# Kernel tuning notes

Hardware: AMD Instinct MI355X
Metric: run time of the kernel (lower is better)

## Reference

```python
import jax, jax.numpy as jnp
import numpy as np

EPS = 1e-10

def _iou(a, b):
    """IoU for boxes in (cx, cy, w, h) format; a, b: (..., 4)."""
    a_min = a[..., :2] - a[..., 2:] * 0.5
    a_max = a[..., :2] + a[..., 2:] * 0.5
    b_min = b[..., :2] - b[..., 2:] * 0.5
    b_max = b[..., :2] + b[..., 2:] * 0.5
    inter_wh = jnp.clip(jnp.minimum(a_max, b_max) - jnp.maximum(a_min, b_min), 0.0)
    inter = inter_wh[..., 0] * inter_wh[..., 1]
    area_a = a[..., 2] * a[..., 3]
    area_b = b[..., 2] * b[..., 3]
    return inter / (area_a + area_b - inter + EPS)

def setup_inputs() -> dict:
    key = jax.random.key(0)
    k1, k2, k3 = jax.random.split(key, 3)
    BATCH, S, C = 16384, 7, 30
    # uniform in (0.01, 1) so sqrt() of w,h channels is finite/differentiable
    preds = jax.random.uniform(k1, (BATCH, S, S, C), jnp.float32, 0.01, 1.0)
    labels = jax.random.uniform(k2, (BATCH, S, S, C), jnp.float32, 0.01, 1.0)
    obj = jax.random.bernoulli(k3, 0.15, (BATCH, S, S)).astype(jnp.float32)
    labels = labels.at[..., 4].set(obj)  # code branches on labels[...,4] == 1
    return {"preds": preds, "labels": labels}

def reference(preds, labels):
    batch = preds.shape[0]
    obj = labels[..., 4] == 1.0  # (B, S, S)
    # faithful quirk: label bbox x-coord is read transposed (labels[i, y, x, 0])
    lb0 = jnp.swapaxes(labels[..., 0], 1, 2)
    lbox = jnp.stack([lb0, labels[..., 1], labels[..., 2], labels[..., 3]], axis=-1)
    iou1 = _iou(preds[..., 0:4], lbox)
    iou2 = _iou(preds[..., 5:9], lbox)
    choose1 = iou1 > iou2
    # branch where box 1 is responsible
    b1 = (5.0 * jnp.sum((preds[..., 0:2] - labels[..., 0:2]) ** 2, -1)
          + jnp.sum((jnp.sqrt(preds[..., 2:4]) - jnp.sqrt(labels[..., 2:4])) ** 2, -1)
          + (iou1 - preds[..., 4]) ** 2
          + 0.5 * preds[..., 9] ** 2)
    # branch where box 2 is responsible (targets read from labels[...,5:9] as in source)
    b2 = (5.0 * jnp.sum((preds[..., 5:7] - labels[..., 5:7]) ** 2, -1)
          + jnp.sum((jnp.sqrt(preds[..., 7:9]) - jnp.sqrt(labels[..., 7:9])) ** 2, -1)
          + (iou2 - preds[..., 9]) ** 2
          + 0.5 * preds[..., 4] ** 2)
    cls = jnp.sum((labels[..., 10:] - preds[..., 10:]) ** 2, -1)
    obj_loss = jnp.where(choose1, b1, b2) + cls
    noobj_loss = 0.5 * (preds[..., 4] ** 2 + preds[..., 9] ** 2)
    total = jnp.sum(jnp.where(obj, obj_loss, noobj_loss))
    return total / batch
```

## Files before the change

kernel.cpp:

```cpp
#include <hip/hip_runtime.h>


#define BATCH 16384
#define S 7
#define C 30
#define NCELLS (BATCH * S * S)
#define BLOCK 256
#define NBLK (NCELLS / BLOCK)

__device__ __forceinline__ float sq(float v) { return v * v; }

__device__ __forceinline__ float iou_box(float acx, float acy, float aw, float ah,
                                         float bcx, float bcy, float bw, float bh) {
    float ax0 = acx - aw * 0.5f, ax1 = acx + aw * 0.5f;
    float ay0 = acy - ah * 0.5f, ay1 = acy + ah * 0.5f;
    float bx0 = bcx - bw * 0.5f, bx1 = bcx + bw * 0.5f;
    float by0 = bcy - bh * 0.5f, by1 = bcy + bh * 0.5f;
    float iw = fmaxf(fminf(ax1, bx1) - fmaxf(ax0, bx0), 0.0f);
    float ih = fmaxf(fminf(ay1, by1) - fmaxf(ay0, by0), 0.0f);
    float inter = iw * ih;
    float denom = aw * ah + bw * bh - inter + 1e-10f;
    return inter / denom;
}

__global__ __launch_bounds__(BLOCK) void yolo_partial_kernel(
        const float* __restrict__ preds,
        const float* __restrict__ labels,
        float* __restrict__ partials) {
    const int tid  = threadIdx.x;
    const int cell = blockIdx.x * BLOCK + tid;

    const float* p = preds  + (size_t)cell * C;
    const float* l = labels + (size_t)cell * C;

    float2 l45 = *reinterpret_cast<const float2*>(l + 4);
    float2 p45 = *reinterpret_cast<const float2*>(p + 4);
    float2 p89 = *reinterpret_cast<const float2*>(p + 8);

    float loss;
    if (l45.x == 1.0f) {
        float2 p01 = *reinterpret_cast<const float2*>(p + 0);
        float2 p23 = *reinterpret_cast<const float2*>(p + 2);
        float2 p67 = *reinterpret_cast<const float2*>(p + 6);
        float2 l01 = *reinterpret_cast<const float2*>(l + 0);
        float2 l23 = *reinterpret_cast<const float2*>(l + 2);
        float2 l67 = *reinterpret_cast<const float2*>(l + 6);
        float2 l89 = *reinterpret_cast<const float2*>(l + 8);

        int b   = cell / (S * S);
        int rem = cell - b * (S * S);
        int y   = rem / S;
        int x   = rem - y * S;
        int pc  = b * (S * S) + x * S + y;
        float lb0 = labels[(size_t)pc * C];

        float iou1 = iou_box(p01.x, p01.y, p23.x, p23.y, lb0, l01.y, l23.x, l23.y);
        float iou2 = iou_box(p45.y, p67.x, p67.y, p89.x, lb0, l01.y, l23.x, l23.y);

        float b1 = 5.0f * (sq(p01.x - l01.x) + sq(p01.y - l01.y))
                 + sq(sqrtf(p23.x) - sqrtf(l23.x)) + sq(sqrtf(p23.y) - sqrtf(l23.y))
                 + sq(iou1 - p45.x)
                 + 0.5f * p89.y * p89.y;

        float b2 = 5.0f * (sq(p45.y - l45.y) + sq(p67.x - l67.x))
                 + sq(sqrtf(p67.y) - sqrtf(l67.y)) + sq(sqrtf(p89.x) - sqrtf(l89.x))
                 + sq(iou2 - p89.y)
                 + 0.5f * p45.x * p45.x;

        float cls = 0.0f;
        #pragma unroll
        for (int i = 0; i < 10; ++i) {
            float2 pc2 = *reinterpret_cast<const float2*>(p + 10 + 2 * i);
            float2 lc2 = *reinterpret_cast<const float2*>(l + 10 + 2 * i);
            cls += sq(lc2.x - pc2.x) + sq(lc2.y - pc2.y);
        }

        loss = ((iou1 > iou2) ? b1 : b2) + cls;
    } else {
        loss = 0.5f * (p45.x * p45.x + p89.y * p89.y);
    }

    #pragma unroll
    for (int off = 32; off > 0; off >>= 1)
        loss += __shfl_down(loss, off, 64);

    __shared__ float wsum[BLOCK / 64];
    int lane = tid & 63;
    int wv   = tid >> 6;
    if (lane == 0) wsum[wv] = loss;
    __syncthreads();
    if (tid == 0) {
        partials[blockIdx.x] = wsum[0] + wsum[1] + wsum[2] + wsum[3];
    }
}

__global__ __launch_bounds__(BLOCK) void yolo_reduce_kernel(
        const float* __restrict__ partials,
        float* __restrict__ out) {
    const int tid = threadIdx.x;
    float s = 0.0f;
    for (int i = tid; i < NBLK; i += BLOCK) s += partials[i];

    #pragma unroll
    for (int off = 32; off > 0; off >>= 1)
        s += __shfl_down(s, off, 64);

    __shared__ float wsum[BLOCK / 64];
    int lane = tid & 63;
    int wv   = tid >> 6;
    if (lane == 0) wsum[wv] = s;
    __syncthreads();
    if (tid == 0) {
        out[0] = (wsum[0] + wsum[1] + wsum[2] + wsum[3]) * (1.0f / (float)BATCH);
    }
}

extern "C" void kernel_launch(void* const* d_in, const int* in_sizes, int n_in,
                              void* d_out, int out_size, void* d_ws, size_t ws_size,
                              hipStream_t stream) {
    const float* preds  = (const float*)d_in[0];
    const float* labels = (const float*)d_in[1];
    float* out = (float*)d_out;
    float* partials = (float*)d_ws;

    yolo_partial_kernel<<<NBLK, BLOCK, 0, stream>>>(preds, labels, partials);
    yolo_reduce_kernel<<<1, BLOCK, 0, stream>>>(partials, out);
}
```

Baseline: 208.4 us.

## Split no-object term into streaming float4 presum kernel over all preds

Adds a kernel that reads preds as fully coalesced float4 and sums 0.5*p4^2 + 0.5*p9^2 for every cell, using a bitmask to pick channels 4 and 9 from each 60-float period. The object kernel then loads only the label's confidence channel up front and returns zero for empty cells. Object cells add a correction that cancels the no-object term. The goal is to swap the scattered strided loads of p4/p9 in every cell for a sequential stream, at the cost of reading all of preds and adding an extra kernel launch.

Result: slower. 214.5 us (+2.9%).

```diff
diff --git a/kernel.cpp b/kernel.cpp
--- a/kernel.cpp
+++ b/kernel.cpp
@@ -6,7 +6,10 @@
 #define C 30
 #define NCELLS (BATCH * S * S)
 #define BLOCK 256
-#define NBLK (NCELLS / BLOCK)
+#define NBLK1 (NCELLS / BLOCK)
+#define NF4P  (NCELLS * C / 4)
+#define K0_BLOCKS 1470
+#define K0_ITERS 16
 
 __device__ __forceinline__ float sq(float v) { return v * v; }
 
@@ -23,7 +26,49 @@
     return inter / denom;
 }
 
-__global__ __launch_bounds__(BLOCK) void yolo_partial_kernel(
+__global__ __launch_bounds__(BLOCK) void yolo_presum_kernel(
+        const float4* __restrict__ preds4,
+        float* __restrict__ partials) {
+    const int tid = blockIdx.x * BLOCK + threadIdx.x;
+    const int stride = K0_BLOCKS * BLOCK;
+    float a0 = 0.f, a1 = 0.f, a2 = 0.f, a3 = 0.f;
+    #pragma unroll
+    for (int k = 0; k < K0_ITERS; k += 4) {
+        int i0 = tid + (k + 0) * stride;
+        int i1 = tid + (k + 1) * stride;
+        int i2 = tid + (k + 2) * stride;
+        int i3 = tid + (k + 3) * stride;
+        float4 v0 = preds4[i0];
+        float4 v1 = preds4[i1];
+        float4 v2 = preds4[i2];
+        float4 v3 = preds4[i3];
+        unsigned s0 = (unsigned)((0x8400000210ull >> (4 * (i0 % 15))) & 15ull);
+        unsigned s1 = (unsigned)((0x8400000210ull >> (4 * (i1 % 15))) & 15ull);
+        unsigned s2 = (unsigned)((0x8400000210ull >> (4 * (i2 % 15))) & 15ull);
+        unsigned s3 = (unsigned)((0x8400000210ull >> (4 * (i3 % 15))) & 15ull);
+        a0 += ((s0 & 1u) ? 0.5f * v0.x * v0.x : 0.f) + ((s0 & 2u) ? 0.5f * v0.y * v0.y : 0.f)
+            + ((s0 & 4u) ? 0.5f * v0.z * v0.z : 0.f) + ((s0 & 8u) ? 0.5f * v0.w * v0.w : 0.f);
+        a1 += ((s1 & 1u) ? 0.5f * v1.x * v1.x : 0.f) + ((s1 & 2u) ? 0.5f * v1.y * v1.y : 0.f)
+            + ((s1 & 4u) ? 0.5f * v1.z * v1.z : 0.f) + ((s1 & 8u) ? 0.5f * v1.w * v1.w : 0.f);
+        a2 += ((s2 & 1u) ? 0.5f * v2.x * v2.x : 0.f) + ((s2 & 2u) ? 0.5f * v2.y * v2.y : 0.f)
+            + ((s2 & 4u) ? 0.5f * v2.z * v2.z : 0.f) + ((s2 & 8u) ? 0.5f * v2.w * v2.w : 0.f);
+        a3 += ((s3 & 1u) ? 0.5f * v3.x * v3.x : 0.f) + ((s3 & 2u) ? 0.5f * v3.y * v3.y : 0.f)
+            + ((s3 & 4u) ? 0.5f * v3.z * v3.z : 0.f) + ((s3 & 8u) ? 0.5f * v3.w * v3.w : 0.f);
+    }
+    float acc = (a0 + a1) + (a2 + a3);
+
+    #pragma unroll
+    for (int off = 32; off > 0; off >>= 1)
+        acc += __shfl_down(acc, off, 64);
+    __shared__ float wsum[BLOCK / 64];
+    int lane = threadIdx.x & 63, wv = threadIdx.x >> 6;
+    if (lane == 0) wsum[wv] = acc;
+    __syncthreads();
+    if (threadIdx.x == 0)
+        partials[blockIdx.x] = wsum[0] + wsum[1] + wsum[2] + wsum[3];
+}
+
+__global__ __launch_bounds__(BLOCK) void yolo_obj_kernel(
         const float* __restrict__ preds,
         const float* __restrict__ labels,
         float* __restrict__ partials) {
@@ -33,17 +78,17 @@
     const float* p = preds  + (size_t)cell * C;
     const float* l = labels + (size_t)cell * C;
 
-    float2 l45 = *reinterpret_cast<const float2*>(l + 4);
-    float2 p45 = *reinterpret_cast<const float2*>(p + 4);
-    float2 p89 = *reinterpret_cast<const float2*>(p + 8);
-
-    float loss;
-    if (l45.x == 1.0f) {
+    float l4 = l[4];
+    float loss = 0.0f;
+    if (l4 == 1.0f) {
         float2 p01 = *reinterpret_cast<const float2*>(p + 0);
         float2 p23 = *reinterpret_cast<const float2*>(p + 2);
+        float2 p45 = *reinterpret_cast<const float2*>(p + 4);
         float2 p67 = *reinterpret_cast<const float2*>(p + 6);
+        float2 p89 = *reinterpret_cast<const float2*>(p + 8);
         float2 l01 = *reinterpret_cast<const float2*>(l + 0);
         float2 l23 = *reinterpret_cast<const float2*>(l + 2);
+        float2 l45 = *reinterpret_cast<const float2*>(l + 4);
         float2 l67 = *reinterpret_cast<const float2*>(l + 6);
         float2 l89 = *reinterpret_cast<const float2*>(l + 8);
 
@@ -57,15 +102,14 @@
         float iou1 = iou_box(p01.x, p01.y, p23.x, p23.y, lb0, l01.y, l23.x, l23.y);
         float iou2 = iou_box(p45.y, p67.x, p67.y, p89.x, lb0, l01.y, l23.x, l23.y);
 
-        float b1 = 5.0f * (sq(p01.x - l01.x) + sq(p01.y - l01.y))
-                 + sq(sqrtf(p23.x) - sqrtf(l23.x)) + sq(sqrtf(p23.y) - sqrtf(l23.y))
-                 + sq(iou1 - p45.x)
-                 + 0.5f * p89.y * p89.y;
-
-        float b2 = 5.0f * (sq(p45.y - l45.y) + sq(p67.x - l67.x))
-                 + sq(sqrtf(p67.y) - sqrtf(l67.y)) + sq(sqrtf(p89.x) - sqrtf(l89.x))
-                 + sq(iou2 - p89.y)
-                 + 0.5f * p45.x * p45.x;
+        float rest1 = 5.0f * (sq(p01.x - l01.x) + sq(p01.y - l01.y))
+                    + sq(sqrtf(p23.x) - sqrtf(l23.x)) + sq(sqrtf(p23.y) - sqrtf(l23.y))
+                    + sq(iou1 - p45.x)
+                    - 0.5f * p45.x * p45.x;
+        float rest2 = 5.0f * (sq(p45.y - l45.y) + sq(p67.x - l67.x))
+                    + sq(sqrtf(p67.y) - sqrtf(l67.y)) + sq(sqrtf(p89.x) - sqrtf(l89.x))
+                    + sq(iou2 - p89.y)
+                    - 0.5f * p89.y * p89.y;
 
         float cls = 0.0f;
         #pragma unroll
@@ -75,44 +119,37 @@
             cls += sq(lc2.x - pc2.x) + sq(lc2.y - pc2.y);
         }
 
-        loss = ((iou1 > iou2) ? b1 : b2) + cls;
-    } else {
-        loss = 0.5f * (p45.x * p45.x + p89.y * p89.y);
+        loss = ((iou1 > iou2) ? rest1 : rest2) + cls;
     }
 
     #pragma unroll
     for (int off = 32; off > 0; off >>= 1)
         loss += __shfl_down(loss, off, 64);
-
     __shared__ float wsum[BLOCK / 64];
-    int lane = tid & 63;
-    int wv   = tid >> 6;
+    int lane = tid & 63, wv = tid >> 6;
     if (lane == 0) wsum[wv] = loss;
     __syncthreads();
-    if (tid == 0) {
+    if (tid == 0)
         partials[blockIdx.x] = wsum[0] + wsum[1] + wsum[2] + wsum[3];
-    }
 }
 
 __global__ __launch_bounds__(BLOCK) void yolo_reduce_kernel(
-        const float* __restrict__ partials,
+        const float* __restrict__ ws,
         float* __restrict__ out) {
     const int tid = threadIdx.x;
     float s = 0.0f;
-    for (int i = tid; i < NBLK; i += BLOCK) s += partials[i];
+    for (int i = tid; i < NBLK1; i += BLOCK)     s += ws[i];
+    for (int i = tid; i < K0_BLOCKS; i += BLOCK) s += ws[NBLK1 + i];
 
     #pragma unroll
     for (int off = 32; off > 0; off >>= 1)
         s += __shfl_down(s, off, 64);
-
     __shared__ float wsum[BLOCK / 64];
-    int lane = tid & 63;
-    int wv   = tid >> 6;
+    int lane = tid & 63, wv = tid >> 6;
     if (lane == 0) wsum[wv] = s;
     __syncthreads();
-    if (tid == 0) {
+    if (tid == 0)
         out[0] = (wsum[0] + wsum[1] + wsum[2] + wsum[3]) * (1.0f / (float)BATCH);
-    }
 }
 
 extern "C" void kernel_launch(void* const* d_in, const int* in_sizes, int n_in,
@@ -121,8 +158,10 @@
     const float* preds  = (const float*)d_in[0];
     const float* labels = (const float*)d_in[1];
     float* out = (float*)d_out;
-    float* partials = (float*)d_ws;
+    float* ws  = (float*)d_ws;
 
-    yolo_partial_kernel<<<NBLK, BLOCK, 0, stream>>>(preds, labels, partials);
-    yolo_reduce_kernel<<<1, BLOCK, 0, stream>>>(partials, out);
+    yolo_presum_kernel<<<K0_BLOCKS, BLOCK, 0, stream>>>(
+        reinterpret_cast<const float4*>(preds), ws + NBLK1);
+    yolo_obj_kernel<<<NBLK1, BLOCK, 0, stream>>>(preds, labels, ws);
+    yolo_reduce_kernel<<<1, BLOCK, 0, stream>>>(ws, out);
 }
```
